# Kernel optimization log

Hardware: AMD Instinct MI355X
Metric: run time of the kernel (lower is better)

## Reference

```python
import jax, jax.numpy as jnp
import numpy as np
import math

TAU = math.log(2.0)   # C=2
LAM = 0.25
BATCH_SIZE = 12


def _lambertw(y, iters=20):
    """Principal-branch Lambert W for y >= -1/e via Halley iteration (on-device,
    replacing the scipy CPU roundtrip)."""
    # initial guess: series expansion near the branch point, log1p elsewhere
    w = jnp.where(
        y < 1.0,
        -1.0 + jnp.sqrt(jnp.maximum(2.0 * (jnp.e * y + 1.0), 0.0)),
        jnp.log1p(y),
    )

    def body(w, _):
        ew = jnp.exp(w)
        f = w * ew - y
        denom = ew * (w + 1.0) - (w + 2.0) * f / (2.0 * (w + 1.0) + 1e-12)
        w = jnp.where(jnp.abs(f) > 0.0, w - f / denom, w)
        return w, None

    w, _ = jax.lax.scan(body, w, None, length=iters)
    return w


def setup_inputs() -> dict:
    key = jax.random.key(0)
    n = 2097152  # rows per label group
    logits = jax.random.normal(key, (3 * n, 3), dtype=jnp.float32)
    return {"discriminator_out": logits, "n0": n, "n1": n, "n2": n}


def reference(discriminator_out, n0, n1, n2):
    # labels: n0 zeros, n1 ones, n2 twos (static sizes)
    labels = jnp.concatenate([
        jnp.zeros((n0,), jnp.int32),
        jnp.ones((n1,), jnp.int32),
        jnp.full((n2,), 2, jnp.int32),
    ])
    # per-row cross entropy (single log_softmax shared by both CE uses in the torch code)
    logp = jax.nn.log_softmax(discriminator_out, axis=-1)
    l_i = -jnp.take_along_axis(logp, labels[:, None], axis=1)[:, 0]  # [N]

    # sigma uses detached losses
    l_det = jax.lax.stop_gradient(l_i)
    y = 0.5 * jnp.maximum(-2.0 / jnp.e, (l_det - TAU) / LAM)  # y >= -1/e
    w = _lambertw(y)
    sigma = jnp.exp(-w)  # log(sigma) = -w

    loss = ((l_i - TAU) * sigma + LAM * jnp.square(w)).sum() / BATCH_SIZE
    return loss
```

## Files before the change

### kernel.cpp

```cpp
#include <hip/hip_runtime.h>
#include <math.h>

#define TAU_C      0.69314718055994530942f
#define LAM_C      0.25f
#define INV_LAM_C  4.0f
#define NEG2_E     -0.73575888234288464320f
#define EULER_E    2.71828182845904523536f
#define INV_BATCH  (1.0f / 12.0f)

#define TBL_N      4096
#define TBL_LMAX   16.0f
#define TBL_SCALE  (TBL_N / TBL_LMAX)

__global__ __launch_bounds__(256) void superloss_table(float* __restrict__ table) {
    int i = blockIdx.x * blockDim.x + threadIdx.x;
    if (i > TBL_N) return;
    float l = (float)i * (TBL_LMAX / TBL_N);

    float y = 0.5f * fmaxf(NEG2_E, (l - TAU_C) * INV_LAM_C);

    float w = (y < 1.0f)
        ? (-1.0f + sqrtf(fmaxf(2.0f * (EULER_E * y + 1.0f), 0.0f)))
        : logf(1.0f + y);

#pragma unroll
    for (int it = 0; it < 8; ++it) {
        float ew  = expf(w);
        float f   = fmaf(w, ew, -y);
        float wp1 = w + 1.0f;
        float num = 2.0f * f * wp1;
        float den = fmaf(2.0f * ew, wp1 * wp1, -(w + 2.0f) * f);
        float wn  = w - num / (den + 1e-30f);
        w = (f != 0.0f) ? wn : w;
    }

    float sigma = expf(-w);
    table[i] = fmaf(l - TAU_C, sigma, LAM_C * w * w);
}

__shared__ float s_tbl[TBL_N + 1];

__device__ __forceinline__ float row_fast(float a, float b, float c, int label) {
    float s  = __expf(a) + __expf(b) + __expf(c);
    float xl = (label == 0) ? a : ((label == 1) ? b : c);
    float l  = __logf(s) - xl;

    float u = l * TBL_SCALE;
    u = fminf(fmaxf(u, 0.0f), (float)TBL_N - 0.001f);
    int   i = (int)u;
    float f = u - (float)i;
    float t0 = s_tbl[i];
    float t1 = s_tbl[i + 1];
    return fmaf(f, t1 - t0, t0);
}

__device__ __forceinline__ float block_reduce(float acc) {
#pragma unroll
    for (int off = 32; off > 0; off >>= 1)
        acc += __shfl_down(acc, off, 64);
    __shared__ float sacc[4];
    int lane = threadIdx.x & 63;
    int wv   = threadIdx.x >> 6;
    if (lane == 0) sacc[wv] = acc;
    __syncthreads();
    float s = 0.0f;
    if (threadIdx.x == 0)
        s = sacc[0] + sacc[1] + sacc[2] + sacc[3];
    return s;
}

__global__ __launch_bounds__(256) void superloss_partial(
        const float* __restrict__ x,
        const float* __restrict__ gtbl,
        const int* __restrict__ pn0,
        const int* __restrict__ pn1,
        float* __restrict__ partial,
        int nrows) {
    for (int i = threadIdx.x; i <= TBL_N; i += 256)
        s_tbl[i] = gtbl[i];
    __syncthreads();

    const int n0  = *pn0;
    const int n01 = n0 + *pn1;

    const int nq     = nrows >> 2;
    const int gid    = blockIdx.x * blockDim.x + threadIdx.x;
    const int stride = gridDim.x * blockDim.x;

    float acc = 0.0f;

    for (int q = gid; q < nq; q += stride) {
        const float4* p = (const float4*)x + 3 * (size_t)q;
        float4 f0 = p[0];
        float4 f1 = p[1];
        float4 f2 = p[2];
        int r0 = q << 2;
        int l0 = (r0     >= n0) + (r0     >= n01);
        int l1 = (r0 + 1 >= n0) + (r0 + 1 >= n01);
        int l2 = (r0 + 2 >= n0) + (r0 + 2 >= n01);
        int l3 = (r0 + 3 >= n0) + (r0 + 3 >= n01);
        acc += row_fast(f0.x, f0.y, f0.z, l0);
        acc += row_fast(f0.w, f1.x, f1.y, l1);
        acc += row_fast(f1.z, f1.w, f2.x, l2);
        acc += row_fast(f2.y, f2.z, f2.w, l3);
    }

    for (int r = (nq << 2) + gid; r < nrows; r += stride) {
        float a = x[3 * (size_t)r];
        float b = x[3 * (size_t)r + 1];
        float c = x[3 * (size_t)r + 2];
        int lab = (r >= n0) + (r >= n01);
        acc += row_fast(a, b, c, lab);
    }

    float s = block_reduce(acc);
    if (threadIdx.x == 0)
        partial[blockIdx.x] = s;
}

__global__ __launch_bounds__(256) void superloss_final(
        const float* __restrict__ partial,
        int np,
        float* __restrict__ out) {
    float acc = 0.0f;
    for (int i = threadIdx.x; i < np; i += 256)
        acc += partial[i];
    float s = block_reduce(acc);
    if (threadIdx.x == 0)
        out[0] = s * INV_BATCH;
}

extern "C" void kernel_launch(void* const* d_in, const int* in_sizes, int n_in,
                              void* d_out, int out_size, void* d_ws, size_t ws_size,
                              hipStream_t stream) {
    const float* x   = (const float*)d_in[0];
    const int*   pn0 = (const int*)d_in[1];
    const int*   pn1 = (const int*)d_in[2];

    const int nrows = in_sizes[0] / 3;

    float* gtbl    = (float*)d_ws;
    float* partial = (float*)d_ws + (TBL_N + 4);

    int nblk = 2048;
    size_t need = (size_t)(TBL_N + 4 + nblk) * sizeof(float);
    if (ws_size < need) {
        nblk = (int)(ws_size / sizeof(float)) - (TBL_N + 4);
        if (nblk < 1) nblk = 1;
    }

    superloss_table<<<(TBL_N + 256) / 256, 256, 0, stream>>>(gtbl);
    superloss_partial<<<nblk, 256, 0, stream>>>(x, gtbl, pn0, pn1, partial, nrows);
    superloss_final<<<1, 256, 0, stream>>>(partial, nblk, (float*)d_out);
}
```

Before: 112.3 us.

## Fuse final reduction via atomics, pack table as float2 pairs, compute knots in double

```diff
diff --git a/kernel.cpp b/kernel.cpp
--- a/kernel.cpp
+++ b/kernel.cpp
@@ -3,78 +3,69 @@
 
 #define TAU_C      0.69314718055994530942f
 #define LAM_C      0.25f
-#define INV_LAM_C  4.0f
-#define NEG2_E     -0.73575888234288464320f
-#define EULER_E    2.71828182845904523536f
+#define NEG_INV_E  -0.36787944117144232160
 #define INV_BATCH  (1.0f / 12.0f)
 
-#define TBL_N      4096
+#define TBL_N      2048
 #define TBL_LMAX   16.0f
 #define TBL_SCALE  (TBL_N / TBL_LMAX)
+#define L0_D       0.50925752433880320442
 
-__global__ __launch_bounds__(256) void superloss_table(float* __restrict__ table) {
-    int i = blockIdx.x * blockDim.x + threadIdx.x;
-    if (i > TBL_N) return;
-    float l = (float)i * (TBL_LMAX / TBL_N);
-
-    float y = 0.5f * fmaxf(NEG2_E, (l - TAU_C) * INV_LAM_C);
-
-    float w = (y < 1.0f)
-        ? (-1.0f + sqrtf(fmaxf(2.0f * (EULER_E * y + 1.0f), 0.0f)))
-        : logf(1.0f + y);
-
+__device__ double lambertw_d(double y) {
+    double w = (y < 1.0)
+        ? (-1.0 + sqrt(fmax(2.0 * (2.718281828459045235 * y + 1.0), 0.0)))
+        : log1p(y);
 #pragma unroll
-    for (int it = 0; it < 8; ++it) {
-        float ew  = expf(w);
-        float f   = fmaf(w, ew, -y);
-        float wp1 = w + 1.0f;
-        float num = 2.0f * f * wp1;
-        float den = fmaf(2.0f * ew, wp1 * wp1, -(w + 2.0f) * f);
-        float wn  = w - num / (den + 1e-30f);
-        w = (f != 0.0f) ? wn : w;
+    for (int it = 0; it < 12; ++it) {
+        double ew  = exp(w);
+        double f   = fma(w, ew, -y);
+        double wp1 = w + 1.0;
+        double den = ew * wp1 - (w + 2.0) * f / (2.0 * wp1 + 1e-300);
+        double wn  = w - f / den;
+        w = (f != 0.0) ? wn : w;
     }
-
-    float sigma = expf(-w);
-    table[i] = fmaf(l - TAU_C, sigma, LAM_C * w * w);
+    return w;
 }
 
-__shared__ float s_tbl[TBL_N + 1];
+__device__ double F_knot(double l) {
+    if (l < L0_D)
+        return 2.718281828459045235 * (l - 0.69314718055994530942) + 0.25;
+    double y = 2.0 * (l - 0.69314718055994530942);
+    double w = lambertw_d(fmax(y, NEG_INV_E));
+    return 0.5 * w + 0.25 * w * w;
+}
+
+__global__ __launch_bounds__(256) void superloss_table(float2* __restrict__ tbl,
+                                                       float* __restrict__ out) {
+    int i = blockIdx.x * blockDim.x + threadIdx.x;
+    if (i == 0) out[0] = 0.0f;
+    if (i > TBL_N) return;
+    double h  = (double)TBL_LMAX / TBL_N;
+    double f0 = F_knot(i * h);
+    double f1 = F_knot((i + 1) * h);
+    tbl[i] = make_float2((float)f0, (float)f1);
+}
+
+__shared__ float2 s_tbl[TBL_N + 1];
 
 __device__ __forceinline__ float row_fast(float a, float b, float c, int label) {
     float s  = __expf(a) + __expf(b) + __expf(c);
     float xl = (label == 0) ? a : ((label == 1) ? b : c);
     float l  = __logf(s) - xl;
 
-    float u = l * TBL_SCALE;
-    u = fminf(fmaxf(u, 0.0f), (float)TBL_N - 0.001f);
+    float u = fminf(fmaxf(l * TBL_SCALE, 0.0f), (float)TBL_N - 0.001f);
     int   i = (int)u;
     float f = u - (float)i;
-    float t0 = s_tbl[i];
-    float t1 = s_tbl[i + 1];
-    return fmaf(f, t1 - t0, t0);
+    float2 t = s_tbl[i];
+    return fmaf(f, t.y - t.x, t.x);
 }
 
-__device__ __forceinline__ float block_reduce(float acc) {
-#pragma unroll
-    for (int off = 32; off > 0; off >>= 1)
-        acc += __shfl_down(acc, off, 64);
-    __shared__ float sacc[4];
-    int lane = threadIdx.x & 63;
-    int wv   = threadIdx.x >> 6;
-    if (lane == 0) sacc[wv] = acc;
-    __syncthreads();
-    float s = 0.0f;
-    if (threadIdx.x == 0)
-        s = sacc[0] + sacc[1] + sacc[2] + sacc[3];
-    return s;
-}
-
-__global__ __launch_bounds__(256) void superloss_partial(
+__global__ __launch_bounds__(256, 8) void superloss_partial(
         const float* __restrict__ x,
-        const float* __restrict__ gtbl,
+        const float2* __restrict__ gtbl,
         const int* __restrict__ pn0,
         const int* __restrict__ pn1,
-        float* __restrict__ partial,
+        float* __restrict__ out,
         int nrows) {
     for (int i = threadIdx.x; i <= TBL_N; i += 256)
         s_tbl[i] = gtbl[i];
@@ -113,21 +104,18 @@
         acc += row_fast(a, b, c, lab);
     }
 
-    float s = block_reduce(acc);
-    if (threadIdx.x == 0)
-        partial[blockIdx.x] = s;
-}
-
-__global__ __launch_bounds__(256) void superloss_final(
-        const float* __restrict__ partial,
-        int np,
-        float* __restrict__ out) {
-    float acc = 0.0f;
-    for (int i = threadIdx.x; i < np; i += 256)
-        acc += partial[i];
-    float s = block_reduce(acc);
-    if (threadIdx.x == 0)
-        out[0] = s * INV_BATCH;
+#pragma unroll
+    for (int off = 32; off > 0; off >>= 1)
+        acc += __shfl_down(acc, off, 64);
+    __shared__ float sacc[4];
+    int lane = threadIdx.x & 63;
+    int wv   = threadIdx.x >> 6;
+    if (lane == 0) sacc[wv] = acc;
+    __syncthreads();
+    if (threadIdx.x == 0) {
+        float s = (sacc[0] + sacc[1] + sacc[2] + sacc[3]) * INV_BATCH;
+        atomicAdd(out, s);
+    }
 }
 
 extern "C" void kernel_launch(void* const* d_in, const int* in_sizes, int n_in,
@@ -139,17 +127,9 @@
 
     const int nrows = in_sizes[0] / 3;
 
-    float* gtbl    = (float*)d_ws;
-    float* partial = (float*)d_ws + (TBL_N + 4);
+    float2* gtbl = (float2*)d_ws;
+    float*  out  = (float*)d_out;
 
-    int nblk = 2048;
-    size_t need = (size_t)(TBL_N + 4 + nblk) * sizeof(float);
-    if (ws_size < need) {
-        nblk = (int)(ws_size / sizeof(float)) - (TBL_N + 4);
-        if (nblk < 1) nblk = 1;
-    }
-
-    superloss_table<<<(TBL_N + 256) / 256, 256, 0, stream>>>(gtbl);
-    superloss_partial<<<nblk, 256, 0, stream>>>(x, gtbl, pn0, pn1, partial, nrows);
-    superloss_final<<<1, 256, 0, stream>>>(partial, nblk, (float*)d_out);
+    superloss_table<<<(TBL_N + 256) / 256, 256, 0, stream>>>(gtbl, out);
+    superloss_partial<<<2048, 256, 0, stream>>>(x, gtbl, pn0, pn1, out, nrows);
 }
```

Result: slower. 131.6 us (+17.2%).

## Precompute loss lookup table at compile time in constant memory

Applied to the files above, without the earlier changes.

```diff
diff --git a/kernel.cpp b/kernel.cpp
--- a/kernel.cpp
+++ b/kernel.cpp
@@ -1,51 +1,77 @@
 #include <hip/hip_runtime.h>
 #include <math.h>
 
-#define TAU_C      0.69314718055994530942f
-#define LAM_C      0.25f
-#define INV_LAM_C  4.0f
-#define NEG2_E     -0.73575888234288464320f
-#define EULER_E    2.71828182845904523536f
-#define INV_BATCH  (1.0f / 12.0f)
+#define TBL_N     1024
+#define KIDX      44.36141955583649f
+#define LOG2E     1.44269504088896340736f
+#define INV_BATCH (1.0f / 12.0f)
 
-#define TBL_N      4096
-#define TBL_LMAX   16.0f
-#define TBL_SCALE  (TBL_N / TBL_LMAX)
+struct TblData { float v[TBL_N + 1]; };
 
-__global__ __launch_bounds__(256) void superloss_table(float* __restrict__ table) {
-    int i = blockIdx.x * blockDim.x + threadIdx.x;
-    if (i > TBL_N) return;
-    float l = (float)i * (TBL_LMAX / TBL_N);
+constexpr double k_ln2 = 0.69314718055994530942;
+constexpr double k_e   = 2.71828182845904523536;
 
-    float y = 0.5f * fmaxf(NEG2_E, (l - TAU_C) * INV_LAM_C);
-
-    float w = (y < 1.0f)
-        ? (-1.0f + sqrtf(fmaxf(2.0f * (EULER_E * y + 1.0f), 0.0f)))
-        : logf(1.0f + y);
-
-#pragma unroll
-    for (int it = 0; it < 8; ++it) {
-        float ew  = expf(w);
-        float f   = fmaf(w, ew, -y);
-        float wp1 = w + 1.0f;
-        float num = 2.0f * f * wp1;
-        float den = fmaf(2.0f * ew, wp1 * wp1, -(w + 2.0f) * f);
-        float wn  = w - num / (den + 1e-30f);
-        w = (f != 0.0f) ? wn : w;
+constexpr double cexp(double x) {
+    double t = x * 1.44269504088896340736;
+    int n = (int)(t + (t >= 0 ? 0.5 : -0.5));
+    double r = x - (double)n * k_ln2;
+    double s = 1.0, term = 1.0;
+    for (int i = 1; i <= 13; ++i) { term *= r / i; s += term; }
+    double p = 1.0;
+    if (n >= 0) for (int i = 0; i <  n; ++i) p *= 2.0;
+    else        for (int i = 0; i < -n; ++i) p *= 0.5;
+    return s * p;
+}
+constexpr double csqrt_(double x) {
+    double r = x > 1.0 ? x : 1.0;
+    for (int i = 0; i < 24; ++i) r = 0.5 * (r + x / r);
+    return r;
+}
+constexpr double clog_(double x) {
+    int n = 0; double m = x;
+    while (m >= 2.0) { m *= 0.5; ++n; }
+    while (m <  1.0) { m *= 2.0; --n; }
+    double z = (m - 1.0) / (m + 1.0), z2 = z * z, s = 0.0, t = z;
+    for (int i = 0; i < 17; ++i) { s += t / (2 * i + 1); t *= z2; }
+    return 2.0 * s + (double)n * k_ln2;
+}
+constexpr TblData make_table() {
+    TblData T{};
+    for (int i = 0; i <= TBL_N; ++i) {
+        double l   = (double)i * (16.0 / TBL_N);
+        double tau = k_ln2;
+        double l0  = tau - 1.0 / (2.0 * k_e);
+        double F;
+        if (l < l0) {
+            F = k_e * (l - tau) + 0.25;
+        } else {
+            double y = 2.0 * (l - tau);
+            double ylim = -1.0 / k_e;
+            if (y < ylim) y = ylim;
+            double w = (y < 3.0) ? (csqrt_(2.0 * (k_e * y + 1.0)) - 1.0)
+                                 : clog_(y);
+            for (int it = 0; it < 4; ++it) {
+                double ew  = cexp(w);
+                double f   = w * ew - y;
+                double wp1 = w + 1.0;
+                double den = ew * wp1 - (w + 2.0) * f / (2.0 * wp1 + 1e-300);
+                if (f != 0.0) w -= f / den;
+            }
+            F = 0.25 * ((1.0 + w) * (1.0 + w) - 1.0);
+        }
+        T.v[i] = (float)F;
     }
-
-    float sigma = expf(-w);
-    table[i] = fmaf(l - TAU_C, sigma, LAM_C * w * w);
+    return T;
 }
+__device__ __constant__ TblData c_tbl = make_table();
 
 __shared__ float s_tbl[TBL_N + 1];
 
 __device__ __forceinline__ float row_fast(float a, float b, float c, int label) {
-    float s  = __expf(a) + __expf(b) + __expf(c);
-    float xl = (label == 0) ? a : ((label == 1) ? b : c);
-    float l  = __logf(s) - xl;
-
-    float u = l * TBL_SCALE;
+    float a2 = a * LOG2E, b2 = b * LOG2E, c2 = c * LOG2E;
+    float s  = exp2f(a2) + exp2f(b2) + exp2f(c2);
+    float xl2 = (label == 0) ? a2 : ((label == 1) ? b2 : c2);
+    float u = (__log2f(s) - xl2) * KIDX;
     u = fminf(fmaxf(u, 0.0f), (float)TBL_N - 0.001f);
     int   i = (int)u;
     float f = u - (float)i;
@@ -71,13 +97,12 @@
 
 __global__ __launch_bounds__(256) void superloss_partial(
         const float* __restrict__ x,
-        const float* __restrict__ gtbl,
         const int* __restrict__ pn0,
         const int* __restrict__ pn1,
         float* __restrict__ partial,
         int nrows) {
     for (int i = threadIdx.x; i <= TBL_N; i += 256)
-        s_tbl[i] = gtbl[i];
+        s_tbl[i] = c_tbl.v[i];
     __syncthreads();
 
     const int n0  = *pn0;
@@ -139,17 +164,14 @@
 
     const int nrows = in_sizes[0] / 3;
 
-    float* gtbl    = (float*)d_ws;
-    float* partial = (float*)d_ws + (TBL_N + 4);
-
     int nblk = 2048;
-    size_t need = (size_t)(TBL_N + 4 + nblk) * sizeof(float);
+    size_t need = (size_t)nblk * sizeof(float);
     if (ws_size < need) {
-        nblk = (int)(ws_size / sizeof(float)) - (TBL_N + 4);
+        nblk = (int)(ws_size / sizeof(float));
         if (nblk < 1) nblk = 1;
     }
 
-    superloss_table<<<(TBL_N + 256) / 256, 256, 0, stream>>>(gtbl);
-    superloss_partial<<<nblk, 256, 0, stream>>>(x, gtbl, pn0, pn1, partial, nrows);
+    float* partial = (float*)d_ws;
+    superloss_partial<<<nblk, 256, 0, stream>>>(x, pn0, pn1, partial, nrows);
     superloss_final<<<1, 256, 0, stream>>>(partial, nblk, (float*)d_out);
 }
```

Measured after the change: 107.6 us. 4.2% less time.
